# Kernel tuning notes

Hardware: AMD Instinct MI355X
Metric: run time of the kernel (lower is better)

The kernel has to match this reference:

```python
import jax, jax.numpy as jnp
import numpy as np

WS = 7    # window size
SS = 3    # shift size
NH = 6    # num heads
C = 192   # dim
HID = 768 # mlp hidden = 4*dim


def _rel_index():
    c = np.stack(np.meshgrid(np.arange(WS), np.arange(WS), indexing='ij')).reshape(2, -1)
    r = (c[:, :, None] - c[:, None, :]).transpose(1, 2, 0)
    r[..., 0] += WS - 1
    r[..., 1] += WS - 1
    r[..., 0] *= 2 * WS - 1
    return r.sum(-1)  # (49, 49) int


def _ln(x, g, b):
    m = jnp.mean(x, -1, keepdims=True)
    v = jnp.var(x, -1, keepdims=True)
    return (x - m) / jnp.sqrt(v + 1e-5) * g + b


def _wpart(x):
    B, H, W, c = x.shape
    return x.reshape(B, H // WS, WS, W // WS, WS, c).transpose(0, 1, 3, 2, 4, 5).reshape(-1, WS * WS, c)


def _wrev(w, H, W):
    B = w.shape[0] // ((H // WS) * (W // WS))
    return w.reshape(B, H // WS, W // WS, WS, WS, -1).transpose(0, 1, 3, 2, 4, 5).reshape(B, H, W, -1)


def setup_inputs() -> dict:
    key = jax.random.key(0)
    ks = jax.random.split(key, 40)
    it = iter(range(40))
    def nrm(shape, s=0.02):
        return jax.random.normal(ks[next(it)], shape, jnp.float32) * s
    B, H, W = 16, 56, 56
    L = H * W
    d = dict(se=nrm((B, L, C), 1.0), de=nrm((B, L, C), 1.0), co=nrm((B, L, C), 1.0))
    # shifted-window attention mask, exactly as Swin builds it
    img = np.zeros((1, H, W, 1), np.float32)
    cnt = 0
    for hs in (slice(0, -WS), slice(-WS, -SS), slice(-SS, None)):
        for cs in (slice(0, -WS), slice(-WS, -SS), slice(-SS, None)):
            img[:, hs, cs, :] = cnt
            cnt += 1
    mw = np.asarray(_wpart(jnp.asarray(img))).reshape(-1, WS * WS)  # (nW, 49)
    am = mw[:, None, :] - mw[:, :, None]
    d['mask_matrix'] = jnp.asarray(np.where(am != 0, -100.0, 0.0).astype(np.float32))
    d.update(
        n1se_g=jnp.ones(C), n1se_b=jnp.zeros(C), n1de_g=jnp.ones(C), n1de_b=jnp.zeros(C),
        rpb_table=nrm(((2 * WS - 1) ** 2, NH)),
        vse_w=nrm((2 * C, C)), vse_b=jnp.zeros(C), vde_w=nrm((2 * C, C)), vde_b=jnp.zeros(C),
        qk_w=nrm((C, 2 * C)), qk_b=jnp.zeros(2 * C),
        pse_w=nrm((C, C)), pse_b=jnp.zeros(C), pde_w=nrm((C, C)), pde_b=jnp.zeros(C),
        n2se_g=jnp.ones(C), n2se_b=jnp.zeros(C), n2de_g=jnp.ones(C), n2de_b=jnp.zeros(C),
        mse_w1=nrm((C, HID)), mse_b1=jnp.zeros(HID), mse_w2=nrm((HID, C)), mse_b2=jnp.zeros(C),
        mde_w1=nrm((C, HID)), mde_b1=jnp.zeros(HID), mde_w2=nrm((HID, C)), mde_b2=jnp.zeros(C),
        H=H, W=W)
    return d


def reference(se, de, co, mask_matrix,
              n1se_g, n1se_b, n1de_g, n1de_b, rpb_table,
              vse_w, vse_b, vde_w, vde_b, qk_w, qk_b,
              pse_w, pse_b, pde_w, pde_b,
              n2se_g, n2se_b, n2de_g, n2de_b,
              mse_w1, mse_b1, mse_w2, mse_b2,
              mde_w1, mde_b1, mde_w2, mde_b2,
              H, W):
    B, L, Cd = se.shape
    dh = Cd // NH
    scale = dh ** -0.5
    sc_se, sc_de = se, de
    se_n = _ln(se, n1se_g, n1se_b).reshape(B, H, W, Cd)
    de_n = _ln(de, n1de_g, n1de_b).reshape(B, H, W, Cd)
    co_n = co.reshape(B, H, W, Cd)  # co is not normed in the torch block
    # cyclic shift (H, W divisible by WS -> zero padding)
    se_s = jnp.roll(se_n, (-SS, -SS), (1, 2))
    de_s = jnp.roll(de_n, (-SS, -SS), (1, 2))
    co_s = jnp.roll(co_n, (-SS, -SS), (1, 2))
    sw, dw, cw = _wpart(se_s), _wpart(de_s), _wpart(co_s)  # (B_, N, C)
    B_, N, _ = sw.shape
    v_se = (jnp.concatenate([sw, cw], -1) @ vse_w + vse_b).reshape(B_, N, NH, dh).transpose(0, 2, 1, 3)
    v_de = (jnp.concatenate([dw, cw], -1) @ vde_w + vde_b).reshape(B_, N, NH, dh).transpose(0, 2, 1, 3)
    qk = (cw @ qk_w + qk_b).reshape(B_, N, 2, NH, dh).transpose(2, 0, 3, 1, 4)
    q, k = qk[0] * scale, qk[1]
    attn = jnp.einsum('bhnd,bhmd->bhnm', q, k)  # (B_, NH, N, N)
    bias = rpb_table[_rel_index().reshape(-1)].reshape(N, N, NH).transpose(2, 0, 1)
    attn = attn + bias[None]
    nW = mask_matrix.shape[0]
    attn = (attn.reshape(B_ // nW, nW, NH, N, N) + mask_matrix[None, :, None]).reshape(B_, NH, N, N)
    attn = jax.nn.softmax(attn, -1)
    se_o = jnp.einsum('bhnm,bhmd->bhnd', attn, v_se).transpose(0, 2, 1, 3).reshape(B_, N, Cd) @ pse_w + pse_b
    de_o = jnp.einsum('bhnm,bhmd->bhnd', attn, v_de).transpose(0, 2, 1, 3).reshape(B_, N, Cd) @ pde_w + pde_b
    se_r = jnp.roll(_wrev(se_o, H, W), (SS, SS), (1, 2)).reshape(B, L, Cd)
    de_r = jnp.roll(_wrev(de_o, H, W), (SS, SS), (1, 2)).reshape(B, L, Cd)
    se_out = sc_se + se_r
    de_out = sc_de + de_r
    se_out = se_out + (jax.nn.gelu(_ln(se_out, n2se_g, n2se_b) @ mse_w1 + mse_b1, approximate=False) @ mse_w2 + mse_b2)
    de_out = de_out + (jax.nn.gelu(_ln(de_out, n2de_g, n2de_b) @ mde_w1 + mde_b1, approximate=False) @ mde_w2 + mde_b2)
    return (se_out, de_out)
```

## Files before the change

### kernel.cpp

```cpp
#include <hip/hip_runtime.h>
#include <hip/hip_bf16.h>
#include <math.h>
#include <stdint.h>

typedef __hip_bfloat16 bf16;
typedef __attribute__((ext_vector_type(8))) short short8;
typedef __attribute__((ext_vector_type(4))) float f32x4;

#define B_SZ   16
#define HH     56
#define WW2    56
#define L_TOK  3136
#define C_DIM  192
#define NH_    6
#define DH     32
#define WS_    7
#define SS_    3
#define NW     49
#define NWIN   64
#define BWIN   (B_SZ*NWIN)
#define TOK    (BWIN*NW)
#define HID_   768

__device__ __forceinline__ float b2f(bf16 x){ return __bfloat162float(x); }
__device__ __forceinline__ bf16  f2b(float x){ return __float2bfloat16(x); }
__device__ __forceinline__ short f2bs(float x){ bf16 h = __float2bfloat16(x); return *reinterpret_cast<short*>(&h); }

__device__ __forceinline__ void gload16(const void* g, void* l) {
    __builtin_amdgcn_global_load_lds(
        (const __attribute__((address_space(1))) void*)(uintptr_t)g,
        (__attribute__((address_space(3))) void*)(uintptr_t)l, 16, 0, 0);
}

__device__ __forceinline__ float wave_sum64(float v){
    #pragma unroll
    for (int off = 32; off > 0; off >>= 1) v += __shfl_xor(v, off, 64);
    return v;
}

__global__ void prep_kernel(const float* __restrict__ se, const float* __restrict__ de,
                            const float* __restrict__ co,
                            const float* __restrict__ g1s, const float* __restrict__ b1s,
                            const float* __restrict__ g1d, const float* __restrict__ b1d,
                            bf16* __restrict__ sw, bf16* __restrict__ dw, bf16* __restrict__ cw)
{
    int t   = blockIdx.x;
    int tid = threadIdx.x;
    int b_  = t / NW, n = t % NW;
    int b   = b_ / NWIN, w = b_ % NWIN;
    int wh  = w >> 3, wwi = w & 7;
    int i   = n / WS_, j = n % WS_;
    int hs  = wh*WS_ + i, ws = wwi*WS_ + j;
    int hsrc = hs + SS_; if (hsrc >= HH)  hsrc -= HH;
    int wsrc = ws + SS_; if (wsrc >= WW2) wsrc -= WW2;
    long src = ((long)(b*L_TOK + hsrc*WW2 + wsrc)) * C_DIM;
    long dst = (long)t * C_DIM;

    {
        float x0 = se[src+tid], x1 = se[src+tid+64], x2 = se[src+tid+128];
        float s  = wave_sum64(x0+x1+x2);
        float ss = wave_sum64(x0*x0 + x1*x1 + x2*x2);
        float mean = s * (1.0f/192.0f);
        float var  = ss * (1.0f/192.0f) - mean*mean;
        float rstd = rsqrtf(var + 1e-5f);
        sw[dst+tid]     = f2b((x0-mean)*rstd*g1s[tid]     + b1s[tid]);
        sw[dst+tid+64]  = f2b((x1-mean)*rstd*g1s[tid+64]  + b1s[tid+64]);
        sw[dst+tid+128] = f2b((x2-mean)*rstd*g1s[tid+128] + b1s[tid+128]);
    }
    {
        float x0 = de[src+tid], x1 = de[src+tid+64], x2 = de[src+tid+128];
        float s  = wave_sum64(x0+x1+x2);
        float ss = wave_sum64(x0*x0 + x1*x1 + x2*x2);
        float mean = s * (1.0f/192.0f);
        float var  = ss * (1.0f/192.0f) - mean*mean;
        float rstd = rsqrtf(var + 1e-5f);
        dw[dst+tid]     = f2b((x0-mean)*rstd*g1d[tid]     + b1d[tid]);
        dw[dst+tid+64]  = f2b((x1-mean)*rstd*g1d[tid+64]  + b1d[tid+64]);
        dw[dst+tid+128] = f2b((x2-mean)*rstd*g1d[tid+128] + b1d[tid+128]);
    }
    cw[dst+tid]     = f2b(co[src+tid]);
    cw[dst+tid+64]  = f2b(co[src+tid+64]);
    cw[dst+tid+128] = f2b(co[src+tid+128]);
}

__global__ __launch_bounds__(256)
void wconv(const float* w0,const float* w1,const float* w2,const float* w3,const float* w4,
           const float* w5,const float* w6,const float* w7,const float* w8, short* dst)
{
    const float* src; int K, N; long doff;
    switch (blockIdx.y) {
      case 0: src=w0; K=384; N=192; doff=0;      break;
      case 1: src=w1; K=384; N=192; doff=73728;  break;
      case 2: src=w2; K=192; N=384; doff=147456; break;
      case 3: src=w3; K=192; N=192; doff=221184; break;
      case 4: src=w4; K=192; N=192; doff=258048; break;
      case 5: src=w5; K=192; N=768; doff=294912; break;
      case 6: src=w6; K=768; N=192; doff=442368; break;
      case 7: src=w7; K=192; N=768; doff=589824; break;
      default:src=w8; K=768; N=192; doff=737280; break;
    }
    int nblk = (K>>5)*(N>>6);
    int bid = blockIdx.x;
    if (bid >= nblk) return;
    int kb = bid / (N>>6), nb = bid % (N>>6);
    __shared__ float tile[32][65];
    int tid = threadIdx.x;
    #pragma unroll
    for (int it = 0; it < 8; ++it) {
        int idx = tid + it*256;
        int r = idx >> 6, c = idx & 63;
        tile[r][c] = src[(long)(kb*32 + r)*N + nb*64 + c];
    }
    __syncthreads();
    int lane = tid & 63, nl = tid >> 6;
    short8 v;
    #pragma unroll
    for (int j = 0; j < 8; ++j)
        v[j] = f2bs(tile[(lane>>4)*8 + j][nl*16 + (lane&15)]);
    long nig = (long)nb*4 + nl;
    *(short8*)(dst + doff + (((long)kb*(N>>4) + nig)*64 + lane)*8) = v;
}

template<int MODE, bool DUAL, int MR16>
__global__ __launch_bounds__(384)
void fgemm2(const bf16* __restrict__ A1, const bf16* __restrict__ A2, int K1, int K,
            const short* __restrict__ wf, const float* __restrict__ bias, int Nn,
            bf16* __restrict__ out, bf16* __restrict__ out2,
            const bf16* __restrict__ A1b, const bf16* __restrict__ A2b,
            const short* __restrict__ wfB, const float* __restrict__ biasB,
            bf16* __restrict__ outB, int nxblk)
{
    __shared__ short AsF[2][MR16][64][8];
    const int MROWS = MR16 * 16;
    const int MPW   = MR16 / 2;
    int tid = threadIdx.x;
    int wid = tid >> 6, lane = tid & 63;
    int wr = (wid >= 3) ? 1 : 0, wc = wid - wr*3;
    int l15 = lane & 15, g = lane >> 4;

    int bx = blockIdx.x;
    const bf16 *A1p = A1, *A2p = A2; const short* wfp = wf;
    const float* biasp = bias; bf16* outp = out;
    if (DUAL && bx >= nxblk) {
        bx -= nxblk; A1p = A1b; A2p = A2b; wfp = wfB; biasp = biasB; outp = outB;
    }
    int row0 = bx * MROWS, col0 = blockIdx.y * 192;
    const int ntiles = Nn >> 4;

    f32x4 acc[MPW][4];
    #pragma unroll
    for (int m = 0; m < MPW; m++)
        #pragma unroll
        for (int n = 0; n < 4; n++)
            acc[m][n] = (f32x4){0.f,0.f,0.f,0.f};

    int nk = K >> 5;
    #define STAGE(buf_, k0_) {                                                   \
        int colk = (k0_) + (g << 3);                                             \
        const bf16* asrc = (colk < K1) ? A1p : A2p;                              \
        int kc = (colk < K1) ? colk : colk - K1;                                 \
        if (wid < MR16)                                                          \
            gload16(asrc + (long)(row0 + wid*16 + l15)*K1 + kc,                  \
                    &AsF[buf_][wid][0][0]);                                      \
        if (MR16 == 8 && wid < 2)                                                \
            gload16(asrc + (long)(row0 + (6+wid)*16 + l15)*K1 + kc,              \
                    &AsF[buf_][(MR16==8 ? 6+wid : 0)][0][0]);                    \
    }

    STAGE(0, 0);
    __syncthreads();
    for (int t = 0; t < nk; ++t) {
        int buf = t & 1;
        if (t + 1 < nk) STAGE(buf ^ 1, (t+1) << 5);
        short8 af[MPW], bf4[4];
        #pragma unroll
        for (int m = 0; m < MPW; m++) af[m] = *((short8*)&AsF[buf][wr*MPW + m][lane][0]);
        const short* wbase = wfp + (((long)t*ntiles + (col0>>4) + wc*4)*64 + lane)*8;
        #pragma unroll
        for (int n = 0; n < 4; n++) bf4[n] = *(const short8*)(wbase + n*512);
        #pragma unroll
        for (int m = 0; m < MPW; m++)
            #pragma unroll
            for (int n = 0; n < 4; n++)
                acc[m][n] = __builtin_amdgcn_mfma_f32_16x16x32_bf16(af[m], bf4[n], acc[m][n], 0, 0, 0);
        __syncthreads();
    }
    #undef STAGE

    #pragma unroll
    for (int m = 0; m < MPW; m++) {
        #pragma unroll
        for (int rr = 0; rr < 4; rr++) {
            int t = row0 + wr*(MROWS/2) + m*16 + g*4 + rr;
            #pragma unroll
            for (int n2 = 0; n2 < 4; n2++) {
                int oc = col0 + wc*64 + n2*16 + l15;
                float v = acc[m][n2][rr] + biasp[oc];
                if (MODE == 0) {
                    outp[(long)t*Nn + oc] = f2b(v);
                } else if (MODE == 1) {
                    int b_ = t / NW, n = t % NW;
                    if (oc < C_DIM) {
                        int head = oc >> 5, d = oc & 31;
                        outp[(((long)b_*NH_ + head)*NW + n)*DH + d] = f2b(v * 0.17677669529663687f);
                    } else {
                        int och = oc - C_DIM;
                        int head = och >> 5, d = och & 31;
                        out2[(((long)b_*NH_ + head)*NW + n)*DH + d] = f2b(v);
                    }
                } else {
                    int b_ = t / NW, n = t % NW;
                    int head = oc >> 5, d = oc & 31;
                    outp[(((long)b_*NH_ + head)*NW + n)*DH + d] = f2b(v);
                }
            }
        }
    }
}

__global__ __launch_bounds__(384)
void pproj_ln2(const bf16* __restrict__ A, const short* __restrict__ wf,
               const float* __restrict__ bias, const float* __restrict__ res,
               const float* __restrict__ g2, const float* __restrict__ b2,
               bf16* __restrict__ x1o, bf16* __restrict__ xno,
               const bf16* __restrict__ Ab, const short* __restrict__ wfB,
               const float* __restrict__ biasB, const float* __restrict__ resB,
               const float* __restrict__ g2B, const float* __restrict__ b2B,
               bf16* __restrict__ x1oB, bf16* __restrict__ xnoB,
               int nxblk)
{
    __shared__ short AsFp[2][8][64][8];
    __shared__ float part[128][3][2];

    int tid = threadIdx.x;
    int wid = tid >> 6, lane = tid & 63;
    int wr = (wid >= 3) ? 1 : 0, wc = wid - wr*3;
    int l15 = lane & 15, g = lane >> 4;

    int bx = blockIdx.x;
    const bf16* Ap = A; const short* wfp = wf; const float* biasp = bias;
    const float* resp = res; const float* g2p = g2; const float* b2p = b2;
    bf16* x1p = x1o; bf16* xnp = xno;
    if (bx >= nxblk) {
        bx -= nxblk; Ap = Ab; wfp = wfB; biasp = biasB; resp = resB;
        g2p = g2B; b2p = b2B; x1p = x1oB; xnp = xnoB;
    }
    int row0 = bx * 128;

    f32x4 acc[4][4];
    #pragma unroll
    for (int m = 0; m < 4; m++)
        #pragma unroll
        for (int n = 0; n < 4; n++)
            acc[m][n] = (f32x4){0.f,0.f,0.f,0.f};

    #define PSTAGE(buf_, k0_) {                                                  \
        int colk = (k0_) + (g << 3);                                             \
        if (wid < 6)                                                             \
            gload16(Ap + (long)(row0 + wid*16 + l15)*C_DIM + colk,               \
                    &AsFp[buf_][wid][0][0]);                                     \
        if (wid < 2)                                                             \
            gload16(Ap + (long)(row0 + (6+wid)*16 + l15)*C_DIM + colk,           \
                    &AsFp[buf_][6+wid][0][0]);                                   \
    }

    PSTAGE(0, 0);
    __syncthreads();
    for (int t = 0; t < 6; ++t) {
        int buf = t & 1;
        if (t + 1 < 6) PSTAGE(buf ^ 1, (t+1) << 5);
        short8 af[4], bf4[4];
        #pragma unroll
        for (int m = 0; m < 4; m++)
            af[m] = *((short8*)&AsFp[buf][wr*4 + m][lane][0]);
        const short* wbase = wfp + (((long)t*12 + wc*4)*64 + lane)*8;
        #pragma unroll
        for (int n = 0; n < 4; n++) bf4[n] = *(const short8*)(wbase + n*512);
        #pragma unroll
        for (int m = 0; m < 4; m++)
            #pragma unroll
            for (int n = 0; n < 4; n++)
                acc[m][n] = __builtin_amdgcn_mfma_f32_16x16x32_bf16(af[m], bf4[n], acc[m][n], 0, 0, 0);
        __syncthreads();
    }
    #undef PSTAGE

    float bias4[4], g24[4], b24[4];
    #pragma unroll
    for (int n2 = 0; n2 < 4; n2++) {
        int oc = wc*64 + n2*16 + l15;
        bias4[n2] = biasp[oc]; g24[n2] = g2p[oc]; b24[n2] = b2p[oc];
    }

    int gtv[4][4];
    #pragma unroll
    for (int m = 0; m < 4; m++) {
        #pragma unroll
        for (int rr = 0; rr < 4; rr++) {
            int t = row0 + wr*64 + m*16 + g*4 + rr;
            int b_ = t / NW, n = t - b_*NW;
            int w = b_ & (NWIN-1), b = b_ >> 6;
            int hs = (w >> 3)*WS_ + n/WS_;
            int wsf = (w & 7)*WS_ + n % WS_;
            int h = hs + SS_;  if (h >= HH)  h -= HH;
            int wc2 = wsf + SS_; if (wc2 >= WW2) wc2 -= WW2;
            int gt = b*L_TOK + h*WW2 + wc2;
            gtv[m][rr] = gt;
            int lrow = wr*64 + m*16 + g*4 + rr;
            float ps = 0.f, pss = 0.f;
            #pragma unroll
            for (int n2 = 0; n2 < 4; n2++) {
                int oc = wc*64 + n2*16 + l15;
                float x1 = resp[(long)gt*C_DIM + oc] + acc[m][n2][rr] + bias4[n2];
                acc[m][n2][rr] = x1;
                x1p[(long)gt*C_DIM + oc] = f2b(x1);
                ps += x1; pss += x1*x1;
            }
            ps  += __shfl_xor(ps, 1);  pss += __shfl_xor(pss, 1);
            ps  += __shfl_xor(ps, 2);  pss += __shfl_xor(pss, 2);
            ps  += __shfl_xor(ps, 4);  pss += __shfl_xor(pss, 4);
            ps  += __shfl_xor(ps, 8);  pss += __shfl_xor(pss, 8);
            if (l15 == 0) {
                part[lrow][wc][0] = ps;
                part[lrow][wc][1] = pss;
            }
        }
    }
    __syncthreads();

    #pragma unroll
    for (int m = 0; m < 4; m++) {
        #pragma unroll
        for (int rr = 0; rr < 4; rr++) {
            int lrow = wr*64 + m*16 + g*4 + rr;
            int gt = gtv[m][rr];
            float s  = part[lrow][0][0] + part[lrow][1][0] + part[lrow][2][0];
            float ss = part[lrow][0][1] + part[lrow][1][1] + part[lrow][2][1];
            float mean = s * (1.0f/192.0f);
            float var  = ss * (1.0f/192.0f) - mean*mean;
            float rstd = rsqrtf(var + 1e-5f);
            #pragma unroll
            for (int n2 = 0; n2 < 4; n2++) {
                int oc = wc*64 + n2*16 + l15;
                xnp[(long)gt*C_DIM + oc] = f2b((acc[m][n2][rr] - mean)*rstd*g24[n2] + b24[n2]);
            }
        }
    }
}

__global__ __launch_bounds__(384)
void mlp_fused2(const bf16* __restrict__ xn, const short* __restrict__ w1f,
                const short* __restrict__ w2f,
                const float* __restrict__ b1, const float* __restrict__ b2,
                const bf16* __restrict__ x1, float* __restrict__ dout,
                const bf16* __restrict__ xnB, const short* __restrict__ w1B,
                const short* __restrict__ w2B,
                const float* __restrict__ b1B, const float* __restrict__ b2B,
                const bf16* __restrict__ x1B, float* __restrict__ doutB,
                int nxblk)
{
    __shared__ short xnF[24*512];
    __shared__ short hidS[24*512];

    int tid = threadIdx.x;
    int wv = tid >> 6, lane = tid & 63;
    int l15 = lane & 15, g = lane >> 4;

    int bx = blockIdx.x;
    const bf16* xnp = xn; const short* w1p = w1f; const short* w2p = w2f;
    const float* b1p = b1; const float* b2p = b2;
    const bf16* x1p = x1; float* doutp = dout;
    if (bx >= nxblk) {
        bx -= nxblk; xnp = xnB; w1p = w1B; w2p = w2B; b1p = b1B; b2p = b2B;
        x1p = x1B; doutp = doutB;
    }
    int row0 = bx * 64;

    #pragma unroll
    for (int p = 0; p < 4; ++p) {
        int pp = wv*4 + p;
        int a = pp / 6, kb = pp % 6;
        gload16(xnp + (long)(row0 + 16*a + l15)*C_DIM + 32*kb + 8*g,
                xnF + (a*6 + kb)*512);
    }
    __syncthreads();

    f32x4 ad[4][2];
    #pragma unroll
    for (int m = 0; m < 4; m++)
        #pragma unroll
        for (int n = 0; n < 2; n++)
            ad[m][n] = (f32x4){0.f,0.f,0.f,0.f};

    for (int s = 0; s < 4; ++s) {
        f32x4 au[4][2];
        #pragma unroll
        for (int m = 0; m < 4; m++)
            #pragma unroll
            for (int n = 0; n < 2; n++)
                au[m][n] = (f32x4){0.f,0.f,0.f,0.f};
        for (int kb = 0; kb < 6; ++kb) {
            short8 af[4];
            #pragma unroll
            for (int m = 0; m < 4; m++) af[m] = *(short8*)(xnF + (m*6 + kb)*512 + lane*8);
            #pragma unroll
            for (int n = 0; n < 2; n++) {
                short8 bfv = *(const short8*)(w1p + (((long)kb*48 + 12*s + 2*wv + n)*64 + lane)*8);
                #pragma unroll
                for (int m = 0; m < 4; m++)
                    au[m][n] = __builtin_amdgcn_mfma_f32_16x16x32_bf16(af[m], bfv, au[m][n], 0, 0, 0);
            }
        }
        __syncthreads();
        #pragma unroll
        for (int n = 0; n < 2; n++) {
            int hc = 32*wv + 16*n + l15;
            float bb = b1p[192*s + hc];
            int kb2 = hc >> 5;
            int Lhi = 16 * ((hc >> 3) & 3);
            int j = hc & 7;
            #pragma unroll
            for (int m = 0; m < 4; m++) {
                #pragma unroll
                for (int rr = 0; rr < 4; rr++) {
                    float v = au[m][n][rr] + bb;
                    float gl = 0.5f * v * (1.0f + erff(v * 0.70710678118654752f));
                    int L = (4*g + rr) + Lhi;
                    hidS[((m*6 + kb2)*64 + L)*8 + j] = f2bs(gl);
                }
            }
        }
        __syncthreads();
        for (int kb = 0; kb < 6; ++kb) {
            short8 hf[4];
            #pragma unroll
            for (int m = 0; m < 4; m++) hf[m] = *(short8*)(hidS + (m*6 + kb)*512 + lane*8);
            #pragma unroll
            for (int n = 0; n < 2; n++) {
                short8 bfv = *(const short8*)(w2p + ((((long)(6*s + kb))*12 + 2*wv + n)*64 + lane)*8);
                #pragma unroll
                for (int m = 0; m < 4; m++)
                    ad[m][n] = __builtin_amdgcn_mfma_f32_16x16x32_bf16(hf[m], bfv, ad[m][n], 0, 0, 0);
            }
        }
    }

    #pragma unroll
    for (int m = 0; m < 4; m++) {
        #pragma unroll
        for (int rr = 0; rr < 4; rr++) {
            int t = row0 + 16*m + 4*g + rr;
            long goff = (long)t*C_DIM;
            #pragma unroll
            for (int n = 0; n < 2; n++) {
                int oc = 32*wv + 16*n + l15;
                float v = ad[m][n][rr] + b2p[oc];
                doutp[goff + oc] = b2f(x1p[goff + oc]) + v;
            }
        }
    }
}

#define BM 128
#define BN 64

template<int MODE>
__global__ __launch_bounds__(256)
void mgemm(const bf16* __restrict__ A1, const bf16* __restrict__ A2, int K1, int K,
           const float* __restrict__ W, const float* __restrict__ bias, int Nn,
           bf16* __restrict__ out, bf16* __restrict__ out2,
           const float* __restrict__ res_src, const bf16* __restrict__ prj,
           int t0, float* __restrict__ dout)
{
    __shared__ short AsF[8][64][8];
    __shared__ short BsF[4][64][8];
    int tid  = threadIdx.x;
    int wid  = tid >> 6, lane = tid & 63;
    int wr   = wid >> 1, wc = wid & 1;
    int row0 = blockIdx.x * BM, col0 = blockIdx.y * BN;

    f32x4 acc[4][2];
    #pragma unroll
    for (int m = 0; m < 4; m++)
        #pragma unroll
        for (int n = 0; n < 2; n++)
            acc[m][n] = (f32x4){0.f, 0.f, 0.f, 0.f};

    int ar = tid >> 2, akseg = tid & 3;
    int bc = tid & 63, bk8 = tid >> 6;

    for (int k0 = 0; k0 < K; k0 += 32) {
        {
            int col = k0 + akseg*8;
            const bf16* asrc = (col < K1) ? A1 : A2;
            int akc = (col < K1) ? col : col - K1;
            #pragma unroll
            for (int rr = 0; rr < 2; rr++) {
                int r = ar + rr*64;
                short8 av = *(const short8*)(asrc + (long)(row0 + r)*K1 + akc);
                *((short8*)&AsF[r >> 4][(r & 15) + (akseg << 4)][0]) = av;
            }
        }
        {
            short8 bv;
            #pragma unroll
            for (int j = 0; j < 8; j++)
                bv[j] = f2bs(W[(long)(k0 + bk8*8 + j)*Nn + col0 + bc]);
            *((short8*)&BsF[bc >> 4][(bc & 15) + (bk8 << 4)][0]) = bv;
        }
        __syncthreads();
        short8 af[4], bfr[2];
        #pragma unroll
        for (int m = 0; m < 4; m++) af[m]  = *((short8*)&AsF[wr*4 + m][lane][0]);
        #pragma unroll
        for (int n = 0; n < 2; n++) bfr[n] = *((short8*)&BsF[wc*2 + n][lane][0]);
        #pragma unroll
        for (int m = 0; m < 4; m++)
            #pragma unroll
            for (int n = 0; n < 2; n++)
                acc[m][n] = __builtin_amdgcn_mfma_f32_16x16x32_bf16(af[m], bfr[n], acc[m][n], 0, 0, 0);
        __syncthreads();
    }

    #pragma unroll
    for (int m = 0; m < 4; m++) {
        #pragma unroll
        for (int rr = 0; rr < 4; rr++) {
            int t = row0 + wr*64 + m*16 + (lane >> 4)*4 + rr;
            if (MODE == 4) {
                int tg = t0 + t;
                int b = tg / L_TOK, l = tg % L_TOK;
                int h = l / WW2, wcol = l % WW2;
                int hp = h - SS_;    if (hp < 0) hp += HH;
                int wp = wcol - SS_; if (wp < 0) wp += WW2;
                int b_ = b*NWIN + (hp/WS_)*8 + (wp/WS_);
                int n  = (hp%WS_)*WS_ + (wp%WS_);
                long wsoff = ((long)b_*NW + n)*C_DIM;
                long goff  = (long)tg*C_DIM;
                #pragma unroll
                for (int n2 = 0; n2 < 2; n2++) {
                    int oc = col0 + wc*32 + n2*16 + (lane & 15);
                    float v = acc[m][n2][rr] + bias[oc];
                    dout[goff + oc] = res_src[goff + oc] + b2f(prj[wsoff + oc]) + v;
                }
            } else {
                #pragma unroll
                for (int n2 = 0; n2 < 2; n2++) {
                    int oc = col0 + wc*32 + n2*16 + (lane & 15);
                    float v = acc[m][n2][rr] + bias[oc];
                    if (MODE == 0) {
                        out[(long)t*Nn + oc] = f2b(v);
                    } else if (MODE == 1) {
                        int b_ = t / NW, n = t % NW;
                        if (oc < C_DIM) {
                            int head = oc >> 5, d = oc & 31;
                            out[(((long)b_*NH_ + head)*NW + n)*DH + d] = f2b(v * 0.17677669529663687f);
                        } else {
                            int och = oc - C_DIM;
                            int head = och >> 5, d = och & 31;
                            out2[(((long)b_*NH_ + head)*NW + n)*DH + d] = f2b(v);
                        }
                    } else if (MODE == 2) {
                        int b_ = t / NW, n = t % NW;
                        int head = oc >> 5, d = oc & 31;
                        out[(((long)b_*NH_ + head)*NW + n)*DH + d] = f2b(v);
                    } else {
                        float g2 = 0.5f * v * (1.0f + erff(v * 0.70710678118654752f));
                        out[(long)t*Nn + oc] = f2b(g2);
                    }
                }
            }
        }
    }
}

#define PSTR 72
#define VSTR 72

__global__ __launch_bounds__(128)
void attn_mfma(const bf16* __restrict__ qb, const bf16* __restrict__ kb,
               const bf16* __restrict__ vse, const bf16* __restrict__ vde,
               const float* __restrict__ rpb,
               bf16* __restrict__ ose, bf16* __restrict__ ode)
{
    __shared__ float rpbs[169*NH_];
    __shared__ short P[2][64][PSTR];
    __shared__ short VTs[2][32][VSTR];
    __shared__ short VTd[2][32][VSTR];
    int tid = threadIdx.x, wid = tid >> 6, lane = tid & 63;
    for (int i = tid; i < 169*NH_; i += 128) rpbs[i] = rpb[i];
    __syncthreads();

    int bh = blockIdx.x*2 + wid;
    int b_ = bh / NH_, head = bh % NH_;
    int w = b_ & (NWIN-1);
    int wh = w >> 3, ww = w & 7;
    long base = (long)bh * (NW*DH);
    int l15 = lane & 15, g = lane >> 4;
    int j0 = lane >> 2, seg = lane & 3;

    short8 qf[4], kf[4], va_[4], vb_[4];
    #pragma unroll
    for (int mi = 0; mi < 4; mi++) {
        int r = l15 + 16*mi; if (r > 48) r = 48;
        qf[mi] = *(const short8*)(qb + base + r*DH + 8*g);
    }
    #pragma unroll
    for (int ni = 0; ni < 4; ni++) {
        int r = l15 + 16*ni; if (r > 48) r = 48;
        kf[ni] = *(const short8*)(kb + base + r*DH + 8*g);
    }
    #pragma unroll
    for (int it = 0; it < 4; ++it) {
        int j = j0 + 16*it;
        va_[it] = (short8){0,0,0,0,0,0,0,0};
        vb_[it] = (short8){0,0,0,0,0,0,0,0};
        if (j < NW) {
            va_[it] = *(const short8*)(vse + base + j*DH + seg*8);
            vb_[it] = *(const short8*)(vde + base + j*DH + seg*8);
        }
    }

    f32x4 sA[4][4];
    #pragma unroll
    for (int mi = 0; mi < 4; mi++)
        #pragma unroll
        for (int ni = 0; ni < 4; ni++)
            sA[mi][ni] = (f32x4){0.f,0.f,0.f,0.f};
    #pragma unroll
    for (int mi = 0; mi < 4; mi++)
        #pragma unroll
        for (int ni = 0; ni < 4; ni++)
            sA[mi][ni] = __builtin_amdgcn_mfma_f32_16x16x32_bf16(qf[mi], kf[ni], sA[mi][ni], 0, 0, 0);

    #pragma unroll
    for (int it = 0; it < 4; ++it) {
        int j = j0 + 16*it;
        #pragma unroll
        for (int s2 = 0; s2 < 8; ++s2) {
            VTs[wid][seg*8 + s2][j] = va_[it][s2];
            VTd[wid][seg*8 + s2][j] = vb_[it][s2];
        }
    }

    int jv[4], j7r_[4], j7c_[4], jrh_[4], jrc_[4];
    #pragma unroll
    for (int ni = 0; ni < 4; ++ni) {
        int j = 16*ni + l15;
        jv[ni] = (j < NW);
        int a = (j*37) >> 8; int c = j - 7*a;
        j7r_[ni] = a; j7c_[ni] = c;
        int jh = wh*7 + a, jw = ww*7 + c;
        jrh_[ni] = (jh >= 49) + (jh >= 53);
        jrc_[ni] = (jw >= 49) + (jw >= 53);
    }

    #pragma unroll
    for (int mi = 0; mi < 4; mi++) {
        #pragma unroll
        for (int rr = 0; rr < 4; rr++) {
            int i = 16*mi + 4*g + rr;
            int iv = (i < NW);
            int i7r = (i*37) >> 8; int i7c = i - 7*i7r;
            int ih = wh*7 + i7r, iw = ww*7 + i7c;
            int irh = (ih >= 49) + (ih >= 53), irc = (iw >= 49) + (iw >= 53);
            float e[4], sum = 0.f;
            #pragma unroll
            for (int ni = 0; ni < 4; ni++) {
                float sv;
                if (iv && jv[ni]) {
                    int ri = (i7r - j7r_[ni] + 6)*13 + (i7c - j7c_[ni] + 6);
                    float msk = (irh == jrh_[ni] && irc == jrc_[ni]) ? 0.f : -100.f;
                    sv = sA[mi][ni][rr] + rpbs[ri*NH_ + head] + msk;
                } else {
                    sv = -1e30f;
                }
                e[ni] = __expf(sv); sum += e[ni];
            }
            sum += __shfl_xor(sum, 1);
            sum += __shfl_xor(sum, 2);
            sum += __shfl_xor(sum, 4);
            sum += __shfl_xor(sum, 8);
            float inv = 1.0f / sum;
            #pragma unroll
            for (int ni = 0; ni < 4; ni++)
                P[wid][i][16*ni + l15] = f2bs(e[ni] * inv);
        }
    }
    __syncthreads();

    f32x4 o1[4][2], o2[4][2];
    #pragma unroll
    for (int mi = 0; mi < 4; mi++)
        #pragma unroll
        for (int di = 0; di < 2; di++) {
            o1[mi][di] = (f32x4){0.f,0.f,0.f,0.f};
            o2[mi][di] = (f32x4){0.f,0.f,0.f,0.f};
        }
    #pragma unroll
    for (int mi = 0; mi < 4; mi++) {
        #pragma unroll
        for (int kk = 0; kk < 2; kk++) {
            short8 ap = *((short8*)&P[wid][16*mi + l15][kk*32 + 8*g]);
            #pragma unroll
            for (int di = 0; di < 2; di++) {
                short8 bv1 = *((short8*)&VTs[wid][16*di + l15][kk*32 + 8*g]);
                o1[mi][di] = __builtin_amdgcn_mfma_f32_16x16x32_bf16(ap, bv1, o1[mi][di], 0, 0, 0);
                short8 bv2 = *((short8*)&VTd[wid][16*di + l15][kk*32 + 8*g]);
                o2[mi][di] = __builtin_amdgcn_mfma_f32_16x16x32_bf16(ap, bv2, o2[mi][di], 0, 0, 0);
            }
        }
    }

    #pragma unroll
    for (int mi = 0; mi < 4; mi++) {
        #pragma unroll
        for (int rr = 0; rr < 4; rr++) {
            int i = 16*mi + 4*g + rr;
            if (i < NW) {
                long ob = ((long)b_*NW + i)*C_DIM + head*DH;
                #pragma unroll
                for (int di = 0; di < 2; di++) {
                    ose[ob + 16*di + l15] = f2b(o1[mi][di][rr]);
                    ode[ob + 16*di + l15] = f2b(o2[mi][di][rr]);
                }
            }
        }
    }
}

__global__ void resid_ln2_kernel(const float* __restrict__ se, const float* __restrict__ de,
                                 const bf16* __restrict__ pse, const bf16* __restrict__ pde,
                                 const float* __restrict__ g2s, const float* __restrict__ bb2s,
                                 const float* __restrict__ g2d, const float* __restrict__ bb2d,
                                 bf16* __restrict__ xns, bf16* __restrict__ xnd)
{
    int t = blockIdx.x, tid = threadIdx.x;
    int b = t / L_TOK, l = t % L_TOK;
    int h = l / WW2, wc = l % WW2;
    int hp = h - SS_;  if (hp < 0) hp += HH;
    int wp = wc - SS_; if (wp < 0) wp += WW2;
    int b_ = b*NWIN + (hp/WS_)*8 + (wp/WS_);
    int n  = (hp%WS_)*WS_ + (wp%WS_);
    long wsoff = ((long)b_*NW + n)*C_DIM;
    long off   = (long)t*C_DIM;
    {
        float x0 = se[off+tid]     + b2f(pse[wsoff+tid]);
        float x1 = se[off+tid+64]  + b2f(pse[wsoff+tid+64]);
        float x2 = se[off+tid+128] + b2f(pse[wsoff+tid+128]);
        float s  = wave_sum64(x0+x1+x2);
        float ss = wave_sum64(x0*x0 + x1*x1 + x2*x2);
        float mean = s * (1.0f/192.0f);
        float var  = ss * (1.0f/192.0f) - mean*mean;
        float rstd = rsqrtf(var + 1e-5f);
        xns[off+tid]     = f2b((x0-mean)*rstd*g2s[tid]     + bb2s[tid]);
        xns[off+tid+64]  = f2b((x1-mean)*rstd*g2s[tid+64]  + bb2s[tid+64]);
        xns[off+tid+128] = f2b((x2-mean)*rstd*g2s[tid+128] + bb2s[tid+128]);
    }
    {
        float x0 = de[off+tid]     + b2f(pde[wsoff+tid]);
        float x1 = de[off+tid+64]  + b2f(pde[wsoff+tid+64]);
        float x2 = de[off+tid+128] + b2f(pde[wsoff+tid+128]);
        float s  = wave_sum64(x0+x1+x2);
        float ss = wave_sum64(x0*x0 + x1*x1 + x2*x2);
        float mean = s * (1.0f/192.0f);
        float var  = ss * (1.0f/192.0f) - mean*mean;
        float rstd = rsqrtf(var + 1e-5f);
        xnd[off+tid]     = f2b((x0-mean)*rstd*g2d[tid]     + bb2d[tid]);
        xnd[off+tid+64]  = f2b((x1-mean)*rstd*g2d[tid+64]  + bb2d[tid+64]);
        xnd[off+tid+128] = f2b((x2-mean)*rstd*g2d[tid+128] + bb2d[tid+128]);
    }
}

extern "C" void kernel_launch(void* const* d_in, const int* in_sizes, int n_in,
                              void* d_out, int out_size, void* d_ws, size_t ws_size,
                              hipStream_t stream)
{
    const float* se     = (const float*)d_in[0];
    const float* de     = (const float*)d_in[1];
    const float* co     = (const float*)d_in[2];
    const float* n1se_g = (const float*)d_in[4];
    const float* n1se_b = (const float*)d_in[5];
    const float* n1de_g = (const float*)d_in[6];
    const float* n1de_b = (const float*)d_in[7];
    const float* rpb    = (const float*)d_in[8];
    const float* vse_w  = (const float*)d_in[9];
    const float* vse_b  = (const float*)d_in[10];
    const float* vde_w  = (const float*)d_in[11];
    const float* vde_b  = (const float*)d_in[12];
    const float* qk_w   = (const float*)d_in[13];
    const float* qk_b   = (const float*)d_in[14];
    const float* pse_w  = (const float*)d_in[15];
    const float* pse_b  = (const float*)d_in[16];
    const float* pde_w  = (const float*)d_in[17];
    const float* pde_b  = (const float*)d_in[18];
    const float* n2se_g = (const float*)d_in[19];
    const float* n2se_b = (const float*)d_in[20];
    const float* n2de_g = (const float*)d_in[21];
    const float* n2de_b = (const float*)d_in[22];
    const float* mse_w1 = (const float*)d_in[23];
    const float* mse_b1 = (const float*)d_in[24];
    const float* mse_w2 = (const float*)d_in[25];
    const float* mse_b2 = (const float*)d_in[26];
    const float* mde_w1 = (const float*)d_in[27];
    const float* mde_b1 = (const float*)d_in[28];
    const float* mde_w2 = (const float*)d_in[29];
    const float* mde_b2 = (const float*)d_in[30];

    char* ws = (char*)d_ws;
    const size_t U = (size_t)TOK * C_DIM * 2;
    bf16* sw   = (bf16*)(ws + 0*U);
    bf16* dw   = (bf16*)(ws + 1*U);
    bf16* cw   = (bf16*)(ws + 2*U);
    bf16* vse  = (bf16*)(ws + 3*U);
    bf16* vde  = (bf16*)(ws + 4*U);
    bf16* ode  = (bf16*)(ws + 5*U);
    bf16* qb   = (bf16*)(ws + 0*U);
    bf16* kb   = (bf16*)(ws + 1*U);
    bf16* ose  = (bf16*)(ws + 2*U);
    bf16* x1se = (bf16*)(ws + 0*U);
    bf16* x1de = (bf16*)(ws + 1*U);
    bf16* xns  = (bf16*)(ws + 3*U);
    bf16* xnd  = (bf16*)(ws + 4*U);
    bf16* fb_pse = (bf16*)(ws + 0*U);
    bf16* fb_pde = (bf16*)(ws + 1*U);
    bf16* fb_xns = (bf16*)(ws + 2*U);
    bf16* fb_xnd = (bf16*)(ws + 3*U);
    bf16* fb_hid = (bf16*)(ws + 4*U);
    short* wfb = (short*)(ws + 6*U);

    const bool frag = (ws_size >= 6*U + 884736ull*2ull);
    float* dout = (float*)d_out;
    const int CH = TOK/2;
    const int NX = TOK/128;

    if (frag)
        wconv<<<dim3(72, 9), 256, 0, stream>>>(vse_w, vde_w, qk_w, pse_w, pde_w,
                                               mse_w1, mse_w2, mde_w1, mde_w2, wfb);
    prep_kernel<<<TOK, 64, 0, stream>>>(se, de, co, n1se_g, n1se_b, n1de_g, n1de_b, sw, dw, cw);

    if (frag) {
        fgemm2<2,true,8><<<dim3(NX*2, 1), 384, 0, stream>>>(sw, cw, C_DIM, 2*C_DIM, wfb + 0, vse_b, C_DIM,
                                                            vse, nullptr,
                                                            dw, cw, wfb + 73728, vde_b, vde, NX);
        fgemm2<1,false,8><<<dim3(NX, 2), 384, 0, stream>>>(cw, cw, C_DIM, C_DIM, wfb + 147456, qk_b, 384,
                                                           qb, kb,
                                                           nullptr, nullptr, nullptr, nullptr, nullptr, 0);
    } else {
        mgemm<2><<<dim3(TOK/BM, C_DIM/BN), 256, 0, stream>>>(sw, cw, C_DIM, 2*C_DIM, vse_w, vse_b, C_DIM,
                                                             vse, nullptr, nullptr, nullptr, 0, nullptr);
        mgemm<2><<<dim3(TOK/BM, C_DIM/BN), 256, 0, stream>>>(dw, cw, C_DIM, 2*C_DIM, vde_w, vde_b, C_DIM,
                                                             vde, nullptr, nullptr, nullptr, 0, nullptr);
        mgemm<1><<<dim3(TOK/BM, 384/BN), 256, 0, stream>>>(cw, cw, C_DIM, C_DIM, qk_w, qk_b, 384,
                                                           qb, kb, nullptr, nullptr, 0, nullptr);
    }

    attn_mfma<<<BWIN*NH_/2, 128, 0, stream>>>(qb, kb, vse, vde, rpb, ose, ode);

    if (frag) {
        pproj_ln2<<<dim3(NX*2, 1), 384, 0, stream>>>(ose, wfb + 221184, pse_b, se, n2se_g, n2se_b,
                                                     x1se, xns,
                                                     ode, wfb + 258048, pde_b, de, n2de_g, n2de_b,
                                                     x1de, xnd, NX);
        mlp_fused2<<<dim3((TOK/64)*2, 1), 384, 0, stream>>>(xns, wfb + 294912, wfb + 442368,
                                                            mse_b1, mse_b2, x1se, dout,
                                                            xnd, wfb + 589824, wfb + 737280,
                                                            mde_b1, mde_b2, x1de,
                                                            dout + (size_t)TOK*C_DIM, TOK/64);
    } else {
        mgemm<0><<<dim3(TOK/BM, C_DIM/BN), 256, 0, stream>>>(ose, ose, C_DIM, C_DIM, pse_w, pse_b, C_DIM,
                                                             fb_pse, nullptr, nullptr, nullptr, 0, nullptr);
        mgemm<0><<<dim3(TOK/BM, C_DIM/BN), 256, 0, stream>>>(ode, ode, C_DIM, C_DIM, pde_w, pde_b, C_DIM,
                                                             fb_pde, nullptr, nullptr, nullptr, 0, nullptr);
        resid_ln2_kernel<<<TOK, 64, 0, stream>>>(se, de, fb_pse, fb_pde,
                                                 n2se_g, n2se_b, n2de_g, n2de_b, fb_xns, fb_xnd);
        for (int c0 = 0; c0 < 2; c0++) {
            int t0 = c0 * CH;
            mgemm<3><<<dim3(CH/BM, HID_/BN), 256, 0, stream>>>(fb_xns + (long)t0*C_DIM, fb_xns + (long)t0*C_DIM,
                                                               C_DIM, C_DIM, mse_w1, mse_b1, HID_,
                                                               fb_hid, nullptr, nullptr, nullptr, 0, nullptr);
            mgemm<4><<<dim3(CH/BM, C_DIM/BN), 256, 0, stream>>>(fb_hid, fb_hid, HID_, HID_, mse_w2, mse_b2, C_DIM,
                                                                nullptr, nullptr, se, fb_pse, t0, dout);
        }
        for (int c0 = 0; c0 < 2; c0++) {
            int t0 = c0 * CH;
            mgemm<3><<<dim3(CH/BM, HID_/BN), 256, 0, stream>>>(fb_xnd + (long)t0*C_DIM, fb_xnd + (long)t0*C_DIM,
                                                               C_DIM, C_DIM, mde_w1, mde_b1, HID_,
                                                               fb_hid, nullptr, nullptr, nullptr, 0, nullptr);
            mgemm<4><<<dim3(CH/BM, C_DIM/BN), 256, 0, stream>>>(fb_hid, fb_hid, HID_, HID_, mde_w2, mde_b2, C_DIM,
                                                                nullptr, nullptr, de, fb_pde, t0,
                                                                dout + (size_t)TOK*C_DIM);
        }
    }
}
```

Measured before the change: 387.3 us.

## Double-buffer MLP hidden slices to overlap up-projection with down-projection

The fused MLP kernel now keeps two shared-memory hidden buffers and runs a software pipeline. The up-projection and GELU for slice s+1 are issued alongside the down-projection for slice s, which cuts the barriers per slice from two to one and lets MFMA work from both GEMMs interleave. Shared memory per block grows from 48KB to 72KB, which may lower occupancy. Full unrolling through macros adds register pressure and code size.

Result: no change. 380.7 us (-1.7%).

```diff
diff --git a/kernel.cpp b/kernel.cpp
--- a/kernel.cpp
+++ b/kernel.cpp
@@ -349,7 +349,7 @@
 }
 
 __global__ __launch_bounds__(384)
-void mlp_fused2(const bf16* __restrict__ xn, const short* __restrict__ w1f,
+void mlp_fused3(const bf16* __restrict__ xn, const short* __restrict__ w1f,
                 const short* __restrict__ w2f,
                 const float* __restrict__ b1, const float* __restrict__ b2,
                 const bf16* __restrict__ x1, float* __restrict__ dout,
@@ -360,7 +360,7 @@
                 int nxblk)
 {
     __shared__ short xnF[24*512];
-    __shared__ short hidS[24*512];
+    __shared__ short hidS[2][24*512];
 
     int tid = threadIdx.x;
     int wv = tid >> 6, lane = tid & 63;
@@ -385,65 +385,93 @@
     }
     __syncthreads();
 
-    f32x4 ad[4][2];
+    f32x4 ad[4][2], au[4][2];
     #pragma unroll
     for (int m = 0; m < 4; m++)
         #pragma unroll
         for (int n = 0; n < 2; n++)
             ad[m][n] = (f32x4){0.f,0.f,0.f,0.f};
 
-    for (int s = 0; s < 4; ++s) {
-        f32x4 au[4][2];
-        #pragma unroll
-        for (int m = 0; m < 4; m++)
-            #pragma unroll
-            for (int n = 0; n < 2; n++)
-                au[m][n] = (f32x4){0.f,0.f,0.f,0.f};
-        for (int kb = 0; kb < 6; ++kb) {
-            short8 af[4];
-            #pragma unroll
-            for (int m = 0; m < 4; m++) af[m] = *(short8*)(xnF + (m*6 + kb)*512 + lane*8);
-            #pragma unroll
-            for (int n = 0; n < 2; n++) {
-                short8 bfv = *(const short8*)(w1p + (((long)kb*48 + 12*s + 2*wv + n)*64 + lane)*8);
-                #pragma unroll
-                for (int m = 0; m < 4; m++)
-                    au[m][n] = __builtin_amdgcn_mfma_f32_16x16x32_bf16(af[m], bfv, au[m][n], 0, 0, 0);
-            }
-        }
-        __syncthreads();
-        #pragma unroll
-        for (int n = 0; n < 2; n++) {
-            int hc = 32*wv + 16*n + l15;
-            float bb = b1p[192*s + hc];
-            int kb2 = hc >> 5;
-            int Lhi = 16 * ((hc >> 3) & 3);
-            int j = hc & 7;
-            #pragma unroll
-            for (int m = 0; m < 4; m++) {
-                #pragma unroll
-                for (int rr = 0; rr < 4; rr++) {
-                    float v = au[m][n][rr] + bb;
-                    float gl = 0.5f * v * (1.0f + erff(v * 0.70710678118654752f));
-                    int L = (4*g + rr) + Lhi;
-                    hidS[((m*6 + kb2)*64 + L)*8 + j] = f2bs(gl);
-                }
-            }
-        }
-        __syncthreads();
-        for (int kb = 0; kb < 6; ++kb) {
-            short8 hf[4];
-            #pragma unroll
-            for (int m = 0; m < 4; m++) hf[m] = *(short8*)(hidS + (m*6 + kb)*512 + lane*8);
-            #pragma unroll
-            for (int n = 0; n < 2; n++) {
-                short8 bfv = *(const short8*)(w2p + ((((long)(6*s + kb))*12 + 2*wv + n)*64 + lane)*8);
-                #pragma unroll
-                for (int m = 0; m < 4; m++)
-                    ad[m][n] = __builtin_amdgcn_mfma_f32_16x16x32_bf16(hf[m], bfv, ad[m][n], 0, 0, 0);
-            }
-        }
-    }
+    #define UP_SLICE(s_) {                                                       \
+        _Pragma("unroll")                                                        \
+        for (int m = 0; m < 4; m++)                                              \
+            _Pragma("unroll")                                                    \
+            for (int n = 0; n < 2; n++)                                          \
+                au[m][n] = (f32x4){0.f,0.f,0.f,0.f};                             \
+        _Pragma("unroll")                                                        \
+        for (int kb = 0; kb < 6; ++kb) {                                         \
+            short8 af[4];                                                        \
+            _Pragma("unroll")                                                    \
+            for (int m = 0; m < 4; m++)                                          \
+                af[m] = *(short8*)(xnF + (m*6 + kb)*512 + lane*8);               \
+            _Pragma("unroll")                                                    \
+            for (int n = 0; n < 2; n++) {                                        \
+                short8 bfv = *(const short8*)(w1p + (((long)kb*48 + 12*(s_) + 2*wv + n)*64 + lane)*8); \
+                _Pragma("unroll")                                                \
+                for (int m = 0; m < 4; m++)                                      \
+                    au[m][n] = __builtin_amdgcn_mfma_f32_16x16x32_bf16(af[m], bfv, au[m][n], 0, 0, 0); \
+            }                                                                    \
+        }                                                                        \
+    }
+
+    #define SCATTER(s_, buf_) {                                                  \
+        _Pragma("unroll")                                                        \
+        for (int n = 0; n < 2; n++) {                                            \
+            int hc = 32*wv + 16*n + l15;                                         \
+            float bb = b1p[192*(s_) + hc];                                       \
+            int kb2 = hc >> 5;                                                   \
+            int Lhi = 16 * ((hc >> 3) & 3);                                      \
+            int j = hc & 7;                                                      \
+            _Pragma("unroll")                                                    \
+            for (int m = 0; m < 4; m++) {                                        \
+                _Pragma("unroll")                                                \
+                for (int rr = 0; rr < 4; rr++) {                                 \
+                    float v = au[m][n][rr] + bb;                                 \
+                    float gl = 0.5f * v * (1.0f + erff(v * 0.70710678118654752f)); \
+                    int L = (4*g + rr) + Lhi;                                    \
+                    hidS[buf_][(m*6 + kb2)*512 + L*8 + j] = f2bs(gl);            \
+                }                                                                \
+            }                                                                    \
+        }                                                                        \
+    }
+
+    #define DOWN_SLICE(s_, buf_) {                                               \
+        _Pragma("unroll")                                                        \
+        for (int kb = 0; kb < 6; ++kb) {                                         \
+            short8 hf[4];                                                        \
+            _Pragma("unroll")                                                    \
+            for (int m = 0; m < 4; m++)                                          \
+                hf[m] = *(short8*)(&hidS[buf_][(m*6 + kb)*512] + lane*8);        \
+            _Pragma("unroll")                                                    \
+            for (int n = 0; n < 2; n++) {                                        \
+                short8 bfv = *(const short8*)(w2p + ((((long)(6*(s_) + kb))*12 + 2*wv + n)*64 + lane)*8); \
+                _Pragma("unroll")                                                \
+                for (int m = 0; m < 4; m++)                                      \
+                    ad[m][n] = __builtin_amdgcn_mfma_f32_16x16x32_bf16(hf[m], bfv, ad[m][n], 0, 0, 0); \
+            }                                                                    \
+        }                                                                        \
+    }
+
+    UP_SLICE(0);
+    SCATTER(0, 0);
+    __syncthreads();
+    UP_SLICE(1);
+    DOWN_SLICE(0, 0);
+    SCATTER(1, 1);
+    __syncthreads();
+    UP_SLICE(2);
+    DOWN_SLICE(1, 1);
+    SCATTER(2, 0);
+    __syncthreads();
+    UP_SLICE(3);
+    DOWN_SLICE(2, 0);
+    SCATTER(3, 1);
+    __syncthreads();
+    DOWN_SLICE(3, 1);
+
+    #undef UP_SLICE
+    #undef SCATTER
+    #undef DOWN_SLICE
 
     #pragma unroll
     for (int m = 0; m < 4; m++) {
@@ -862,7 +890,7 @@
                                                      x1se, xns,
                                                      ode, wfb + 258048, pde_b, de, n2de_g, n2de_b,
                                                      x1de, xnd, NX);
-        mlp_fused2<<<dim3((TOK/64)*2, 1), 384, 0, stream>>>(xns, wfb + 294912, wfb + 442368,
+        mlp_fused3<<<dim3((TOK/64)*2, 1), 384, 0, stream>>>(xns, wfb + 294912, wfb + 442368,
                                                             mse_b1, mse_b2, x1se, dout,
                                                             xnd, wfb + 589824, wfb + 737280,
                                                             mde_b1, mde_b2, x1de,
```
